# Optimization experiments

Measured on AMD Instinct MI355X. Metric: run time of the kernel, lower is better.

## Reference

```python
import jax, jax.numpy as jnp
import numpy as np
import math

C = 512
GROUPS = 32
EPS = 1e-06


def group_norm(x, w, b):
    # x: [B, C, H, W]; 32 groups over channels
    B, Cc, H, W = x.shape
    xg = x.reshape(B, GROUPS, Cc // GROUPS, H, W)
    mu = jnp.mean(xg, axis=(2, 3, 4), keepdims=True)
    var = jnp.var(xg, axis=(2, 3, 4), keepdims=True)
    xn = ((xg - mu) * jax.lax.rsqrt(var + EPS)).reshape(B, Cc, H, W)
    return xn * w[None, :, None, None] + b[None, :, None, None]


def setup_inputs() -> dict:
    key = jax.random.key(0)
    ks = jax.random.split(key, 7)
    B, H, W = 2, 64, 64
    x = jax.random.normal(ks[0], (B, C, H, W), dtype=jnp.float32)
    gn_w = jnp.ones((C,), dtype=jnp.float32)
    gn_b = jnp.zeros((C,), dtype=jnp.float32)
    s = 1.0 / math.sqrt(C)
    qkv_w = jax.random.normal(ks[1], (3 * C, C), dtype=jnp.float32) * s
    qkv_b = jnp.zeros((3 * C,), dtype=jnp.float32)
    proj_w = jax.random.normal(ks[2], (C, C), dtype=jnp.float32) * s
    proj_b = jnp.zeros((C,), dtype=jnp.float32)
    return {"x": x, "gn_w": gn_w, "gn_b": gn_b, "qkv_w": qkv_w,
            "qkv_b": qkv_b, "proj_w": proj_w, "proj_b": proj_b}


def reference(x, gn_w, gn_b, qkv_w, qkv_b, proj_w, proj_b):
    residue = x
    B, Cc, H, W = x.shape
    N = H * W
    constant = 1.0 / math.sqrt(Cc)
    xn = group_norm(x, gn_w, gn_b)
    # 1x1 conv == channel matmul
    qkv = jnp.einsum('bchw,oc->bohw', xn, qkv_w) + qkv_b[None, :, None, None]
    q, k, v = jnp.split(qkv, 3, axis=1)
    q = q.reshape(B, Cc, N)
    k = k.reshape(B, Cc, N)
    v = v.reshape(B, Cc, N)
    # attn[b,i,j] = sum_c k[b,c,i] * q[b,c,j]   (k^T @ q, per original code)
    attn = jnp.einsum('bci,bcj->bij', k, q) * constant
    soft = jax.nn.softmax(attn, axis=2)  # softmax over q-index j, as in torch dim=2
    # output[b,c,i] = sum_j v[b,c,j] * soft[b,j,i]   (v @ soft)
    out = jnp.einsum('bcj,bji->bci', v, soft).reshape(B, Cc, H, W)
    proj = jnp.einsum('bchw,oc->bohw', out, proj_w) + proj_b[None, :, None, None]
    return residue + proj
```

## Files before the change

kernel.cpp:

```cpp
#include <hip/hip_runtime.h>
#include <hip/hip_bf16.h>
#include <math.h>

typedef unsigned short ushort_t;
typedef __attribute__((ext_vector_type(8))) unsigned short ushort8;
typedef __attribute__((ext_vector_type(8))) __bf16 bf16x8;
typedef __attribute__((ext_vector_type(4))) float f32x4;

__device__ inline ushort_t f2b(float f) {
  __hip_bfloat16 h = __float2bfloat16(f);
  return __builtin_bit_cast(ushort_t, h);
}
__device__ inline float b2f(ushort_t u) {
  __hip_bfloat16 h = __builtin_bit_cast(__hip_bfloat16, u);
  return __bfloat162float(h);
}

__device__ inline void gload16(const ushort_t* g, ushort_t* l) {
  __builtin_amdgcn_global_load_lds(
      (const __attribute__((address_space(1))) unsigned int*)g,
      (__attribute__((address_space(3))) unsigned int*)l, 16, 0, 0);
}

__device__ inline void xcd_swz(int& bx, int& by, int& bz) {
  const int nx = gridDim.x, ny = gridDim.y;
  const int nwg = nx * ny * gridDim.z;
  const int orig = blockIdx.x + nx * (blockIdx.y + ny * blockIdx.z);
  const int q = nwg >> 3, r = nwg & 7, xcd = orig & 7, loc = orig >> 3;
  const int wg = (xcd < r ? xcd * (q + 1) : r * (q + 1) + (xcd - r) * q) + loc;
  bx = wg % nx;
  by = (wg / nx) % ny;
  bz = wg / (nx * ny);
}

__global__ __launch_bounds__(256) void prep_weights(
    const float* __restrict__ qkv_w, const float* __restrict__ proj_w,
    ushort_t* __restrict__ qkvw, ushort_t* __restrict__ projw) {
  int idx = blockIdx.x * 256 + threadIdx.x;
  const int NQ = 1536 * 512;
  if (idx < NQ) {
    qkvw[idx] = f2b(qkv_w[idx]);
  } else {
    int j = idx - NQ;
    if (j < 512 * 512) projw[j] = f2b(proj_w[j]);
  }
}

__global__ __launch_bounds__(256) void gn_stats(const float* __restrict__ x,
                                                float* __restrict__ stats) {
  const int tid = threadIdx.x;
  const int bg = blockIdx.x;
  const float4* xv = (const float4*)(x + (size_t)bg * 65536);
  float s = 0.f, ss = 0.f;
  for (int i = tid; i < 16384; i += 256) {
    float4 v = xv[i];
    s += v.x + v.y + v.z + v.w;
    ss += v.x * v.x + v.y * v.y + v.z * v.z + v.w * v.w;
  }
  __shared__ float red[8];
  for (int off = 32; off > 0; off >>= 1) {
    s += __shfl_down(s, off);
    ss += __shfl_down(ss, off);
  }
  if ((tid & 63) == 0) { red[tid >> 6] = s; red[4 + (tid >> 6)] = ss; }
  __syncthreads();
  if (tid == 0) {
    float st = red[0] + red[1] + red[2] + red[3];
    float sst = red[4] + red[5] + red[6] + red[7];
    float mean = st * (1.f / 65536.f);
    float var = sst * (1.f / 65536.f) - mean * mean;
    stats[bg * 2] = mean;
    stats[bg * 2 + 1] = rsqrtf(var + 1e-6f);
  }
}

__global__ __launch_bounds__(256) void gn_apply_t(
    const float* __restrict__ x, const float* __restrict__ w,
    const float* __restrict__ bgn, const float* __restrict__ stats,
    ushort_t* __restrict__ xnT) {
  __shared__ ushort_t tile[64][68];
  const int b = blockIdx.z;
  const int p0 = blockIdx.x * 64, c0 = blockIdx.y * 64;
  const int tid = threadIdx.x;
  const float* xb = x + ((size_t)b * 512 + c0) * 4096 + p0;
  const int tc = tid >> 4, tp = (tid & 15) * 4;
#pragma unroll
  for (int pass = 0; pass < 4; ++pass) {
    int c = pass * 16 + tc;
    int cg = c0 + c;
    float mean = stats[(b * 32 + (cg >> 4)) * 2];
    float inv = stats[(b * 32 + (cg >> 4)) * 2 + 1];
    float wc = w[cg] * inv;
    float bc = bgn[cg] - mean * wc;
    float4 v = *(const float4*)(xb + (size_t)c * 4096 + tp);
    tile[c][tp] = f2b(v.x * wc + bc);
    tile[c][tp + 1] = f2b(v.y * wc + bc);
    tile[c][tp + 2] = f2b(v.z * wc + bc);
    tile[c][tp + 3] = f2b(v.w * wc + bc);
  }
  __syncthreads();
  const int c8 = (tid & 7) * 8;
#pragma unroll
  for (int pass = 0; pass < 2; ++pass) {
    int p = pass * 32 + (tid >> 3);
    ushort8 u;
#pragma unroll
    for (int e = 0; e < 8; ++e) u[e] = tile[c8 + e][p];
    *(ushort8*)(xnT + ((size_t)b * 4096 + p0 + p) * 512 + c0 + c8) = u;
  }
}

template <int EPI>
__global__ __launch_bounds__(512, 2) void gemm8(
    const ushort_t* __restrict__ A, const ushort_t* __restrict__ B,
    void* __restrict__ Cg, const float* __restrict__ bias,
    float* __restrict__ smp, int N, int K, int lda, int ldb, size_t sA,
    size_t sB, size_t sC, float scale) {
  __shared__ __align__(16) ushort_t Al[2][256 * 64];
  __shared__ __align__(16) ushort_t Bl[2][256 * 64];
  __shared__ float s_max[2][256], s_sum[2][256];

  int bx, by, bz;
  xcd_swz(bx, by, bz);
  const ushort_t* Ab = A + bz * sA;
  const ushort_t* Bb = B + bz * sB;
  const int bm0 = by * 256, bn0 = bx * 256;
  const int tid = threadIdx.x;
  const int w = tid >> 6, lane = tid & 63;
  const int wr = w >> 2, wc = w & 3;
  const int fr = lane & 15, fq = lane >> 4;

  const int srow = tid >> 3, scb = tid & 7;
  const int ssw = scb ^ (srow & 7);
  const ushort_t* aS = Ab + (size_t)(bm0 + srow) * lda + ssw * 8;
  const ushort_t* bS = Bb + (size_t)(bn0 + srow) * ldb + ssw * 8;

  auto stage_a = [&](int s, int kk) {
#pragma unroll
    for (int g = 0; g < 4; ++g)
      gload16(aS + (size_t)(g * 64) * lda + kk, &Al[s][g * 4096 + w * 512]);
  };
  auto stage_b = [&](int s, int kk) {
#pragma unroll
    for (int g = 0; g < 4; ++g)
      gload16(bS + (size_t)(g * 64) * ldb + kk, &Bl[s][g * 4096 + w * 512]);
  };

  f32x4 acc[8][4] = {};
  bf16x8 a_r[4][2], b_r[4][2];

  auto read_a = [&](int s, int mh) {
#pragma unroll
    for (int mi = 0; mi < 4; ++mi) {
      int row = wr * 128 + mh * 64 + mi * 16 + fr;
#pragma unroll
      for (int ks = 0; ks < 2; ++ks) {
        int blk = ((ks * 4 + fq) ^ (row & 7)) * 8;
        a_r[mi][ks] = *(const bf16x8*)&Al[s][row * 64 + blk];
      }
    }
  };
  auto read_b = [&](int s, int nh) {
#pragma unroll
    for (int ni = 0; ni < 2; ++ni) {
      int row = wc * 64 + nh * 32 + ni * 16 + fr;
#pragma unroll
      for (int ks = 0; ks < 2; ++ks) {
        int blk = ((ks * 4 + fq) ^ (row & 7)) * 8;
        b_r[nh * 2 + ni][ks] = *(const bf16x8*)&Bl[s][row * 64 + blk];
      }
    }
  };
  auto phase_mfma = [&](int mh, int nh) {
    __builtin_amdgcn_s_setprio(1);
#pragma unroll
    for (int ks = 0; ks < 2; ++ks)
#pragma unroll
      for (int mi = 0; mi < 4; ++mi)
#pragma unroll
        for (int ni = 0; ni < 2; ++ni)
          acc[mh * 4 + mi][nh * 2 + ni] =
              __builtin_amdgcn_mfma_f32_16x16x32_bf16(
                  a_r[mi][ks], b_r[nh * 2 + ni][ks],
                  acc[mh * 4 + mi][nh * 2 + ni], 0, 0, 0);
    __builtin_amdgcn_s_setprio(0);
  };

  const int nt = K >> 6;
  stage_b(0, 0);
  stage_a(0, 0);
  if (nt > 1) {
    stage_b(1, 64);
    stage_a(1, 64);
    asm volatile("s_waitcnt vmcnt(8)" ::: "memory");
  } else {
    asm volatile("s_waitcnt vmcnt(0)" ::: "memory");
  }
  __builtin_amdgcn_s_barrier();

  for (int t = 0; t < nt; ++t) {
    const int s = t & 1;
    const int kk2 = (t + 2) << 6;
    const bool st2 = (t + 2) < nt;
    read_a(s, 0);
    read_b(s, 0);
    __builtin_amdgcn_s_barrier();
    phase_mfma(0, 0);
    __builtin_amdgcn_s_barrier();
    read_b(s, 1);
    __builtin_amdgcn_s_barrier();
    phase_mfma(0, 1);
    __builtin_amdgcn_s_barrier();
    read_a(s, 1);
    asm volatile("" ::: "memory");
    if (st2) stage_b(s, kk2);
    __builtin_amdgcn_s_barrier();
    phase_mfma(1, 0);
    __builtin_amdgcn_s_barrier();
    asm volatile("" ::: "memory");
    if (st2) stage_a(s, kk2);
    __builtin_amdgcn_s_barrier();
    phase_mfma(1, 1);
    if (st2)
      asm volatile("s_waitcnt vmcnt(8)" ::: "memory");
    else if (t + 1 < nt)
      asm volatile("s_waitcnt vmcnt(0)" ::: "memory");
    __builtin_amdgcn_s_barrier();
  }

  const size_t cbase = (size_t)bz * sC;
#pragma unroll
  for (int mi = 0; mi < 8; ++mi) {
#pragma unroll
    for (int r = 0; r < 4; ++r) {
      int gm = bm0 + wr * 128 + mi * 16 + fq * 4 + r;
#pragma unroll
      for (int ni = 0; ni < 4; ++ni) {
        int gn = bn0 + wc * 64 + ni * 16 + fr;
        float v = acc[mi][ni][r];
        size_t off = cbase + (size_t)gm * N + gn;
        ((ushort_t*)Cg)[off] = f2b(__expf(fminf(v * scale, 80.f)));
      }
    }
  }

  if constexpr (EPI == 2) {
    float cm[4], cs4[4];
#pragma unroll
    for (int ni = 0; ni < 4; ++ni) {
      float m = -3e38f;
#pragma unroll
      for (int mi = 0; mi < 8; ++mi)
#pragma unroll
        for (int r = 0; r < 4; ++r) m = fmaxf(m, acc[mi][ni][r] * scale);
      m = fmaxf(m, __shfl_xor(m, 16));
      m = fmaxf(m, __shfl_xor(m, 32));
      float s = 0.f;
#pragma unroll
      for (int mi = 0; mi < 8; ++mi)
#pragma unroll
        for (int r = 0; r < 4; ++r) s += __expf(acc[mi][ni][r] * scale - m);
      s += __shfl_xor(s, 16);
      s += __shfl_xor(s, 32);
      cm[ni] = m;
      cs4[ni] = s;
    }
    __syncthreads();
    if (lane < 16) {
#pragma unroll
      for (int ni = 0; ni < 4; ++ni) {
        s_max[wr][wc * 64 + ni * 16 + lane] = cm[ni];
        s_sum[wr][wc * 64 + ni * 16 + lane] = cs4[ni];
      }
    }
    __syncthreads();
    if (tid < 256) {
      float m0 = s_max[0][tid], m1 = s_max[1][tid];
      float M = fmaxf(m0, m1);
      float S = s_sum[0][tid] * __expf(m0 - M) + s_sum[1][tid] * __expf(m1 - M);
      size_t o = (((size_t)bz * 16 + by) * 4096 + bn0 + tid) * 2;
      smp[o] = M;
      smp[o + 1] = S;
    }
  }
}

template <int EPI, int SPLIT>
__global__ __launch_bounds__(256, 2) void gemm_pl(
    const ushort_t* __restrict__ A, const ushort_t* __restrict__ B,
    void* __restrict__ Cg, const float* __restrict__ bias,
    const float* __restrict__ colsc, int N, int K, int lda, int ldb,
    size_t sA, size_t sB, size_t sC, size_t sSp) {
  __shared__ __align__(16) ushort_t Al[2][128 * 64];
  __shared__ __align__(16) ushort_t Bl[2][128 * 64];
  int bx, by, bzt;
  xcd_swz(bx, by, bzt);
  const int bz = bzt / SPLIT, sp = bzt % SPLIT;
  const ushort_t* Ab = A + bz * sA + (size_t)sp * K;
  const ushort_t* Bb = B + bz * sB + (size_t)sp * K;
  const int bm0 = by * 128, bn0 = bx * 128;
  const int tid = threadIdx.x;
  const int w = tid >> 6, lane = tid & 63;
  const int wm = (w >> 1) * 64, wn = (w & 1) * 64;
  const int fr = lane & 15, fq = lane >> 4;

  const int srow = tid >> 3, scb = tid & 7;
  const int ssw = scb ^ (srow & 7);
  const ushort_t* aS = Ab + (size_t)(bm0 + srow) * lda + ssw * 8;
  const ushort_t* bS = Bb + (size_t)(bn0 + srow) * ldb + ssw * 8;

  auto stage = [&](int s, int kk) {
#pragma unroll
    for (int g = 0; g < 4; ++g)
      gload16(aS + (size_t)(g * 32) * lda + kk, &Al[s][g * 2048 + w * 512]);
#pragma unroll
    for (int g = 0; g < 4; ++g)
      gload16(bS + (size_t)(g * 32) * ldb + kk, &Bl[s][g * 2048 + w * 512]);
  };

  f32x4 acc[4][4] = {};
  bf16x8 a_r[4][2], b_r[4][2];

  const int nt = K >> 6;
  stage(0, 0);
  if (nt > 1) {
    stage(1, 64);
    asm volatile("s_waitcnt vmcnt(8)" ::: "memory");
  } else {
    asm volatile("s_waitcnt vmcnt(0)" ::: "memory");
  }
  __builtin_amdgcn_s_barrier();

  for (int t = 0; t < nt; ++t) {
    const int s = t & 1;
#pragma unroll
    for (int mi = 0; mi < 4; ++mi) {
      int row = wm + mi * 16 + fr;
#pragma unroll
      for (int ks = 0; ks < 2; ++ks) {
        int blk = ((ks * 4 + fq) ^ (row & 7)) * 8;
        a_r[mi][ks] = *(const bf16x8*)&Al[s][row * 64 + blk];
      }
    }
#pragma unroll
    for (int ni = 0; ni < 4; ++ni) {
      int row = wn + ni * 16 + fr;
#pragma unroll
      for (int ks = 0; ks < 2; ++ks) {
        int blk = ((ks * 4 + fq) ^ (row & 7)) * 8;
        b_r[ni][ks] = *(const bf16x8*)&Bl[s][row * 64 + blk];
      }
    }
    __builtin_amdgcn_s_barrier();
    __builtin_amdgcn_s_setprio(1);
#pragma unroll
    for (int ks = 0; ks < 2; ++ks)
#pragma unroll
      for (int mi = 0; mi < 4; ++mi)
#pragma unroll
        for (int ni = 0; ni < 2; ++ni)
          acc[mi][ni] = __builtin_amdgcn_mfma_f32_16x16x32_bf16(
              a_r[mi][ks], b_r[ni][ks], acc[mi][ni], 0, 0, 0);
    __builtin_amdgcn_s_setprio(0);
    __builtin_amdgcn_s_barrier();
    if (t + 2 < nt) stage(s, (t + 2) << 6);
    __builtin_amdgcn_s_setprio(1);
#pragma unroll
    for (int ks = 0; ks < 2; ++ks)
#pragma unroll
      for (int mi = 0; mi < 4; ++mi)
#pragma unroll
        for (int ni = 2; ni < 4; ++ni)
          acc[mi][ni] = __builtin_amdgcn_mfma_f32_16x16x32_bf16(
              a_r[mi][ks], b_r[ni][ks], acc[mi][ni], 0, 0, 0);
    __builtin_amdgcn_s_setprio(0);
    if (t + 2 < nt)
      asm volatile("s_waitcnt vmcnt(8)" ::: "memory");
    else if (t + 1 < nt)
      asm volatile("s_waitcnt vmcnt(0)" ::: "memory");
    __builtin_amdgcn_s_barrier();
  }

  const int r0 = (lane >> 4) * 4;
  const size_t cbase = (size_t)sp * sSp + (size_t)bz * sC;
#pragma unroll
  for (int mi = 0; mi < 4; mi++) {
#pragma unroll
    for (int r = 0; r < 4; r++) {
      int gm = bm0 + wm + mi * 16 + r0 + r;
#pragma unroll
      for (int ni = 0; ni < 4; ni++) {
        int gn = bn0 + wn + ni * 16 + fr;
        float v = acc[mi][ni][r];
        size_t off = cbase + (size_t)gm * N + gn;
        if constexpr (EPI == 0) {
          ((ushort_t*)Cg)[off] = f2b(v + bias[gn]);
        } else if constexpr (EPI == 3) {
          ((ushort_t*)Cg)[off] = f2b(v * colsc[(size_t)bz * 4096 + gn]);
        } else {
          ((ushort_t*)Cg)[off] = f2b(v);
        }
      }
    }
  }
}

__global__ __launch_bounds__(256) void sm_fin(const float* __restrict__ part,
                                              float* __restrict__ alpha) {
  int idx = blockIdx.x * 256 + threadIdx.x;
  int b = idx >> 12, j = idx & 4095;
  float M = -3e38f, S = 0.f;
#pragma unroll
  for (int rc = 0; rc < 16; rc++) {
    size_t o = (((size_t)b * 16 + rc) * 4096 + j) * 2;
    float mi = part[o], si = part[o + 1];
    float nm = fmaxf(M, mi);
    S = S * __expf(M - nm) + si * __expf(mi - nm);
    M = nm;
  }
  alpha[idx] = __expf(-M) / S;
}

__global__ __launch_bounds__(256) void finalize(
    const ushort_t* __restrict__ part, const float* __restrict__ x,
    const float* __restrict__ pb, float* __restrict__ out) {
  __shared__ float tile[64][68];
  const int b = blockIdx.z;
  const int p0 = blockIdx.x * 64, o0 = blockIdx.y * 64;
  const int tid = threadIdx.x;
  const int tp = tid >> 2, to = (tid & 3) * 16;
  const size_t base = ((size_t)b * 4096 + p0 + tp) * 512 + o0 + to;
  ushort8 u0 = *(const ushort8*)(part + base);
  ushort8 u1 = *(const ushort8*)(part + base + 8);
  ushort8 v0 = *(const ushort8*)(part + 4194304 + base);
  ushort8 v1 = *(const ushort8*)(part + 4194304 + base + 8);
#pragma unroll
  for (int e = 0; e < 8; ++e) {
    tile[tp][to + e] = b2f(u0[e]) + b2f(v0[e]);
    tile[tp][to + 8 + e] = b2f(u1[e]) + b2f(v1[e]);
  }
  __syncthreads();
  const int wo = tid >> 2, wp = (tid & 3) * 16;
  float bias = pb[o0 + wo];
  const float* xr = x + ((size_t)b * 512 + o0 + wo) * 4096 + p0 + wp;
  float* orow = out + ((size_t)b * 512 + o0 + wo) * 4096 + p0 + wp;
#pragma unroll
  for (int e = 0; e < 16; ++e)
    orow[e] = tile[wp + e][wo] + xr[e] + bias;
}

extern "C" void kernel_launch(void* const* d_in, const int* in_sizes, int n_in,
                              void* d_out, int out_size, void* d_ws,
                              size_t ws_size, hipStream_t stream) {
  const float* x = (const float*)d_in[0];
  const float* gn_w = (const float*)d_in[1];
  const float* gn_b = (const float*)d_in[2];
  const float* qkv_w = (const float*)d_in[3];
  const float* qkv_b = (const float*)d_in[4];
  const float* proj_w = (const float*)d_in[5];
  const float* proj_b = (const float*)d_in[6];
  float* out = (float*)d_out;

  char* ws = (char*)d_ws;
  ushort_t* xnT   = (ushort_t*)(ws);
  ushort_t* Wpp   = (ushort_t*)(ws);
  ushort_t* qkvw  = (ushort_t*)(ws + 8388608);
  ushort_t* projw = (ushort_t*)(ws + 9961472);
  float*    stats = (float*)(ws + 10485760);
  ushort_t* qkvT  = (ushort_t*)(ws + 10486272);
  ushort_t* part  = (ushort_t*)(ws + 10486272);
  ushort_t* P     = (ushort_t*)(ws + 35652096);
  float*    smp   = (float*)(ws + 102760960);
  float*    alpha = (float*)(ws + 104858112);

  const float scale = 0.04419417382415922f;
  const size_t sXN = 2097152, sQKV = (size_t)4096 * 1536, sP = 16777216;

  prep_weights<<<4096, 256, 0, stream>>>(qkv_w, proj_w, qkvw, projw);
  gn_stats<<<64, 256, 0, stream>>>(x, stats);
  gn_apply_t<<<dim3(64, 8, 2), 256, 0, stream>>>(x, gn_w, gn_b, stats, xnT);
  gemm_pl<0, 1><<<dim3(12, 64, 1), 256, 0, stream>>>(
      xnT, qkvw, qkvT, qkv_b, nullptr, 1536, 512, 512, 512, 0, 0, 0, 0);
  gemm8<2><<<dim3(16, 16, 2), 512, 0, stream>>>(
      qkvT, qkvT + 512, P, nullptr, smp, 4096, 512, 1536, 1536, sQKV, sQKV,
      sP, scale);
  sm_fin<<<32, 256, 0, stream>>>(smp, alpha);
  gemm_pl<3, 1><<<dim3(32, 4, 2), 256, 0, stream>>>(
      projw, qkvT + 1024, Wpp, nullptr, alpha, 4096, 512, 512, 1536, 0, sQKV,
      sXN, 0);
  gemm_pl<5, 2><<<dim3(4, 32, 4), 256, 0, stream>>>(
      P, Wpp, part, nullptr, nullptr, 512, 2048, 4096, 4096, sP, sXN, sXN,
      4194304);
  finalize<<<dim3(64, 8, 2), 256, 0, stream>>>(part, x, proj_b, out);
}
```

Measured before the change: 171.7 us.

## Stage exp tile through LDS for coalesced stores and drop softmax max tracking

```diff
diff --git a/kernel.cpp b/kernel.cpp
--- a/kernel.cpp
+++ b/kernel.cpp
@@ -110,15 +110,14 @@
   }
 }
 
-template <int EPI>
 __global__ __launch_bounds__(512, 2) void gemm8(
     const ushort_t* __restrict__ A, const ushort_t* __restrict__ B,
-    void* __restrict__ Cg, const float* __restrict__ bias,
-    float* __restrict__ smp, int N, int K, int lda, int ldb, size_t sA,
-    size_t sB, size_t sC, float scale) {
-  __shared__ __align__(16) ushort_t Al[2][256 * 64];
-  __shared__ __align__(16) ushort_t Bl[2][256 * 64];
-  __shared__ float s_max[2][256], s_sum[2][256];
+    ushort_t* __restrict__ Cg, float* __restrict__ smp, int N, int K, int lda,
+    int ldb, size_t sA, size_t sB, size_t sC, float scale) {
+  __shared__ __align__(16) ushort_t smem[66560];
+  ushort_t* Asl = smem;
+  ushort_t* Bsl = smem + 32768;
+  float* s_sum = (float*)(smem + 65536);
 
   int bx, by, bz;
   xcd_swz(bx, by, bz);
@@ -138,12 +137,14 @@
   auto stage_a = [&](int s, int kk) {
 #pragma unroll
     for (int g = 0; g < 4; ++g)
-      gload16(aS + (size_t)(g * 64) * lda + kk, &Al[s][g * 4096 + w * 512]);
+      gload16(aS + (size_t)(g * 64) * lda + kk,
+              &Asl[s * 16384 + g * 4096 + w * 512]);
   };
   auto stage_b = [&](int s, int kk) {
 #pragma unroll
     for (int g = 0; g < 4; ++g)
-      gload16(bS + (size_t)(g * 64) * ldb + kk, &Bl[s][g * 4096 + w * 512]);
+      gload16(bS + (size_t)(g * 64) * ldb + kk,
+              &Bsl[s * 16384 + g * 4096 + w * 512]);
   };
 
   f32x4 acc[8][4] = {};
@@ -156,7 +157,7 @@
 #pragma unroll
       for (int ks = 0; ks < 2; ++ks) {
         int blk = ((ks * 4 + fq) ^ (row & 7)) * 8;
-        a_r[mi][ks] = *(const bf16x8*)&Al[s][row * 64 + blk];
+        a_r[mi][ks] = *(const bf16x8*)&Asl[s * 16384 + row * 64 + blk];
       }
     }
   };
@@ -167,7 +168,7 @@
 #pragma unroll
       for (int ks = 0; ks < 2; ++ks) {
         int blk = ((ks * 4 + fq) ^ (row & 7)) * 8;
-        b_r[nh * 2 + ni][ks] = *(const bf16x8*)&Bl[s][row * 64 + blk];
+        b_r[nh * 2 + ni][ks] = *(const bf16x8*)&Bsl[s * 16384 + row * 64 + blk];
       }
     }
   };
@@ -227,61 +228,51 @@
       asm volatile("s_waitcnt vmcnt(0)" ::: "memory");
     __builtin_amdgcn_s_barrier();
   }
+  __syncthreads();
 
   const size_t cbase = (size_t)bz * sC;
-#pragma unroll
-  for (int mi = 0; mi < 8; ++mi) {
-#pragma unroll
-    for (int r = 0; r < 4; ++r) {
-      int gm = bm0 + wr * 128 + mi * 16 + fq * 4 + r;
-#pragma unroll
-      for (int ni = 0; ni < 4; ++ni) {
-        int gn = bn0 + wc * 64 + ni * 16 + fr;
-        float v = acc[mi][ni][r];
-        size_t off = cbase + (size_t)gm * N + gn;
-        ((ushort_t*)Cg)[off] = f2b(__expf(fminf(v * scale, 80.f)));
-      }
-    }
-  }
-
-  if constexpr (EPI == 2) {
-    float cm[4], cs4[4];
-#pragma unroll
-    for (int ni = 0; ni < 4; ++ni) {
-      float m = -3e38f;
+  float csum[4] = {0.f, 0.f, 0.f, 0.f};
+  ushort_t* tp = smem;
+#pragma unroll
+  for (int step = 0; step < 2; ++step) {
+    if (wr == step) {
 #pragma unroll
       for (int mi = 0; mi < 8; ++mi)
 #pragma unroll
-        for (int r = 0; r < 4; ++r) m = fmaxf(m, acc[mi][ni][r] * scale);
-      m = fmaxf(m, __shfl_xor(m, 16));
-      m = fmaxf(m, __shfl_xor(m, 32));
-      float s = 0.f;
-#pragma unroll
-      for (int mi = 0; mi < 8; ++mi)
-#pragma unroll
-        for (int r = 0; r < 4; ++r) s += __expf(acc[mi][ni][r] * scale - m);
-      s += __shfl_xor(s, 16);
-      s += __shfl_xor(s, 32);
-      cm[ni] = m;
-      cs4[ni] = s;
+        for (int ni = 0; ni < 4; ++ni)
+#pragma unroll
+          for (int r = 0; r < 4; ++r) {
+            int lr = mi * 16 + fq * 4 + r;
+            int col = wc * 64 + ni * 16 + fr;
+            float e = __expf(fminf(acc[mi][ni][r] * scale, 76.f));
+            csum[ni] += e;
+            int cblk = col >> 3;
+            tp[lr * 256 + (((cblk ^ (lr & 7)) << 3) | (col & 7))] = f2b(e);
+          }
     }
     __syncthreads();
-    if (lane < 16) {
-#pragma unroll
-      for (int ni = 0; ni < 4; ++ni) {
-        s_max[wr][wc * 64 + ni * 16 + lane] = cm[ni];
-        s_sum[wr][wc * 64 + ni * 16 + lane] = cs4[ni];
-      }
+#pragma unroll
+    for (int k = 0; k < 8; ++k) {
+      int row = (tid >> 5) + 16 * k;
+      int cblk = tid & 31;
+      ushort8 u = *(const ushort8*)&tp[row * 256 + ((cblk ^ (row & 7)) << 3)];
+      size_t off =
+          cbase + (size_t)(bm0 + step * 128 + row) * N + bn0 + cblk * 8;
+      *(ushort8*)(Cg + off) = u;
     }
     __syncthreads();
-    if (tid < 256) {
-      float m0 = s_max[0][tid], m1 = s_max[1][tid];
-      float M = fmaxf(m0, m1);
-      float S = s_sum[0][tid] * __expf(m0 - M) + s_sum[1][tid] * __expf(m1 - M);
-      size_t o = (((size_t)bz * 16 + by) * 4096 + bn0 + tid) * 2;
-      smp[o] = M;
-      smp[o + 1] = S;
-    }
+  }
+#pragma unroll
+  for (int ni = 0; ni < 4; ++ni) {
+    float s = csum[ni];
+    s += __shfl_xor(s, 16);
+    s += __shfl_xor(s, 32);
+    if (lane < 16) s_sum[wr * 256 + wc * 64 + ni * 16 + lane] = s;
+  }
+  __syncthreads();
+  if (tid < 256) {
+    smp[((size_t)bz * 16 + by) * 4096 + bn0 + tid] =
+        s_sum[tid] + s_sum[256 + tid];
   }
 }
 
@@ -409,16 +400,11 @@
                                               float* __restrict__ alpha) {
   int idx = blockIdx.x * 256 + threadIdx.x;
   int b = idx >> 12, j = idx & 4095;
-  float M = -3e38f, S = 0.f;
-#pragma unroll
-  for (int rc = 0; rc < 16; rc++) {
-    size_t o = (((size_t)b * 16 + rc) * 4096 + j) * 2;
-    float mi = part[o], si = part[o + 1];
-    float nm = fmaxf(M, mi);
-    S = S * __expf(M - nm) + si * __expf(mi - nm);
-    M = nm;
-  }
-  alpha[idx] = __expf(-M) / S;
+  float S = 0.f;
+#pragma unroll
+  for (int rc = 0; rc < 16; rc++)
+    S += part[((size_t)b * 16 + rc) * 4096 + j];
+  alpha[idx] = 1.f / S;
 }
 
 __global__ __launch_bounds__(256) void finalize(
@@ -481,9 +467,8 @@
   gn_apply_t<<<dim3(64, 8, 2), 256, 0, stream>>>(x, gn_w, gn_b, stats, xnT);
   gemm_pl<0, 1><<<dim3(12, 64, 1), 256, 0, stream>>>(
       xnT, qkvw, qkvT, qkv_b, nullptr, 1536, 512, 512, 512, 0, 0, 0, 0);
-  gemm8<2><<<dim3(16, 16, 2), 512, 0, stream>>>(
-      qkvT, qkvT + 512, P, nullptr, smp, 4096, 512, 1536, 1536, sQKV, sQKV,
-      sP, scale);
+  gemm8<<<dim3(16, 16, 2), 512, 0, stream>>>(
+      qkvT, qkvT + 512, P, smp, 4096, 512, 1536, 1536, sQKV, sQKV, sP, scale);
   sm_fin<<<32, 256, 0, stream>>>(smp, alpha);
   gemm_pl<3, 1><<<dim3(32, 4, 2), 256, 0, stream>>>(
       projw, qkvT + 1024, Wpp, nullptr, alpha, 4096, 512, 512, 1536, 0, sQKV,
```

Result: no change. 172.6 us (+0.5%).
